# Kernel optimization log

Hardware: AMD Instinct MI355X
Metric: run time of the kernel (lower is better)

## Reference

```python
import jax, jax.numpy as jnp
import numpy as np

N, D = 1024, 512
BS, N_TEXT, N_VIDEO = 64, 16, 16
BETA = 1.0
N_ITERS = 50


def setup_inputs() -> dict:
    key = jax.random.key(0)
    k1, k2 = jax.random.split(key)
    return {
        "t_prob": jax.random.normal(k1, (N, D), dtype=jnp.float32),
        "v_prob": jax.random.normal(k2, (N, D), dtype=jnp.float32),
        "n": N,
        "bs": BS,
        "n_text": N_TEXT,
        "n_video": N_VIDEO,
    }


def _l2norm(x):
    # matches F.normalize(x, p=2, dim=1) (eps irrelevant for randn inputs)
    return x / jnp.linalg.norm(x, axis=1, keepdims=True)


def reference(t_prob, v_prob, n, bs, n_text, n_video):
    dt = t_prob.dtype
    x = _l2norm(t_prob)
    y = _l2norm(v_prob)
    C = 1.0 - x @ y.T                      # [n, n] cosine distance
    A = jnp.exp(-C / BETA)

    sigma0 = jnp.ones((n, 1), dtype=dt) / n
    T0 = jnp.ones((n, n), dtype=dt)

    def step(carry, _):
        T, sigma = carry
        Q = A * T                          # [n, n]
        delta = 1.0 / (n * (Q @ sigma))    # [n, 1]
        sigma_new = 1.0 / (n * (Q.T @ delta))  # [n, 1]
        # diag(delta) @ Q @ diag(sigma) == row/col rescale
        T_new = delta * Q * sigma_new.T
        return (T_new, sigma_new), None

    (T, _), _ = jax.lax.scan(step, (T0, sigma0), None, length=N_ITERS)

    distance_matrix = C.T @ T              # [n, n]
    distance_matrix = distance_matrix.reshape(bs, n_text, bs, n_video).mean(axis=(1, 3))
    dis_loss = jnp.trace(distance_matrix)
    return distance_matrix, dis_loss
```

## Files before the change

kernel.cpp:

```cpp
#include <hip/hip_runtime.h>
#include <math.h>


#define NWG 32
#define TPB 256
#define NIT 50
#define NREP 4

typedef unsigned long long ull;

constexpr int CL_OFF   = 0;
constexpr int CVEC_OFF = 1024 * 1024;
constexpr int CNT_OFF  = CVEC_OFF + 3 * NREP * 1024;

__global__ __launch_bounds__(256) void k_gemm(const float* __restrict__ X,
                                              const float* __restrict__ Y,
                                              float* __restrict__ ws) {
    __shared__ float As[32][68];
    __shared__ float Bs[32][68];
    __shared__ float nX[64], nY[64];
    float* Cl = ws + CL_OFF;

    int tid = threadIdx.x;
    int tx = tid & 15, ty = tid >> 4;
    int bx = blockIdx.x, by = blockIdx.y;
    int lr0 = tid >> 3;
    int kq  = (tid & 7) * 4;

    float acc[4][4] = {};
    float sx0 = 0.f, sx1 = 0.f, sy0 = 0.f, sy1 = 0.f;
    for (int k0 = 0; k0 < 512; k0 += 32) {
        float4 xa = *(const float4*)(X + (size_t)(by * 64 + lr0) * 512 + k0 + kq);
        float4 xb = *(const float4*)(X + (size_t)(by * 64 + lr0 + 32) * 512 + k0 + kq);
        float4 ya = *(const float4*)(Y + (size_t)(bx * 64 + lr0) * 512 + k0 + kq);
        float4 yb = *(const float4*)(Y + (size_t)(bx * 64 + lr0 + 32) * 512 + k0 + kq);
        sx0 += xa.x * xa.x + xa.y * xa.y + xa.z * xa.z + xa.w * xa.w;
        sx1 += xb.x * xb.x + xb.y * xb.y + xb.z * xb.z + xb.w * xb.w;
        sy0 += ya.x * ya.x + ya.y * ya.y + ya.z * ya.z + ya.w * ya.w;
        sy1 += yb.x * yb.x + yb.y * yb.y + yb.z * yb.z + yb.w * yb.w;
        As[kq + 0][lr0] = xa.x; As[kq + 1][lr0] = xa.y;
        As[kq + 2][lr0] = xa.z; As[kq + 3][lr0] = xa.w;
        As[kq + 0][lr0 + 32] = xb.x; As[kq + 1][lr0 + 32] = xb.y;
        As[kq + 2][lr0 + 32] = xb.z; As[kq + 3][lr0 + 32] = xb.w;
        Bs[kq + 0][lr0] = ya.x; Bs[kq + 1][lr0] = ya.y;
        Bs[kq + 2][lr0] = ya.z; Bs[kq + 3][lr0] = ya.w;
        Bs[kq + 0][lr0 + 32] = yb.x; Bs[kq + 1][lr0 + 32] = yb.y;
        Bs[kq + 2][lr0 + 32] = yb.z; Bs[kq + 3][lr0 + 32] = yb.w;
        __syncthreads();
#pragma unroll
        for (int kk = 0; kk < 32; ++kk) {
            float4 a4 = *(const float4*)&As[kk][4 * ty];
            float4 b4 = *(const float4*)&Bs[kk][4 * tx];
            float av[4] = {a4.x, a4.y, a4.z, a4.w};
            float bv[4] = {b4.x, b4.y, b4.z, b4.w};
#pragma unroll
            for (int r = 0; r < 4; ++r)
#pragma unroll
                for (int q = 0; q < 4; ++q) acc[r][q] += av[r] * bv[q];
        }
        __syncthreads();
    }
#pragma unroll
    for (int m = 1; m < 8; m <<= 1) {
        sx0 += __shfl_xor(sx0, m, 64);
        sx1 += __shfl_xor(sx1, m, 64);
        sy0 += __shfl_xor(sy0, m, 64);
        sy1 += __shfl_xor(sy1, m, 64);
    }
    if ((tid & 7) == 0) {
        nX[lr0] = sx0; nX[lr0 + 32] = sx1;
        nY[lr0] = sy0; nY[lr0 + 32] = sy1;
    }
    __syncthreads();

    int i0 = by * 64 + 4 * ty, j0 = bx * 64 + 4 * tx;
    float vy[4];
#pragma unroll
    for (int q = 0; q < 4; ++q) vy[q] = 1.0f / sqrtf(nY[4 * tx + q]);
#pragma unroll
    for (int r = 0; r < 4; ++r) {
        float vx = 1.0f / sqrtf(nX[4 * ty + r]);
        float4 o;
        o.x = acc[r][0] * vx * vy[0] - 1.0f;
        o.y = acc[r][1] * vx * vy[1] - 1.0f;
        o.z = acc[r][2] * vx * vy[2] - 1.0f;
        o.w = acc[r][3] * vx * vy[3] - 1.0f;
        *(float4*)(Cl + (size_t)(i0 + r) * 1024 + j0) = o;
    }
}

__global__ __launch_bounds__(256, 1) void k_ipot(float* __restrict__ ws,
                                                 float* __restrict__ out) {
    __shared__ float sL[1024];
    __shared__ float aL[32];
    __shared__ float buf[4 * 1024];
    __shared__ float twv[4];

    const int g = blockIdx.x, tid = threadIdx.x;
    const int rs = tid >> 6, lane = tid & 63;
    float* Cl   = ws + CL_OFF;
    float* cvec = ws + CVEC_OFF;
    unsigned* grp = (unsigned*)(ws + CNT_OFF);

    float C[8][16], E[8][16];
#pragma unroll
    for (int i = 0; i < 8; ++i) {
        const float* src = Cl + (size_t)(g * 32 + rs * 8 + i) * 1024 + lane * 16;
#pragma unroll
        for (int q = 0; q < 4; ++q) {
            float4 c = *(const float4*)(src + 4 * q);
            C[i][4 * q + 0] = c.x; C[i][4 * q + 1] = c.y;
            C[i][4 * q + 2] = c.z; C[i][4 * q + 3] = c.w;
        }
    }
#pragma unroll
    for (int i = 0; i < 8; ++i)
#pragma unroll
        for (int u = 0; u < 16; ++u) E[i][u] = __expf(C[i][u]);

    float bv[4] = {1.0f, 1.0f, 1.0f, 1.0f};

    for (int t = 0; t < NIT; ++t) {
        if (t == 0) {
            *(float4*)&sL[4 * tid] =
                make_float4(1/1024.f, 1/1024.f, 1/1024.f, 1/1024.f);
        } else {
            if (tid == 0) {
                unsigned tgt = (unsigned)t * 8u;
                long gd = 0;
                while (__hip_atomic_load(&grp[0], __ATOMIC_RELAXED, __HIP_MEMORY_SCOPE_AGENT) < tgt ||
                       __hip_atomic_load(&grp[1], __ATOMIC_RELAXED, __HIP_MEMORY_SCOPE_AGENT) < tgt ||
                       __hip_atomic_load(&grp[2], __ATOMIC_RELAXED, __HIP_MEMORY_SCOPE_AGENT) < tgt ||
                       __hip_atomic_load(&grp[3], __ATOMIC_RELAXED, __HIP_MEMORY_SCOPE_AGENT) < tgt) {
                    __builtin_amdgcn_s_sleep(1);
                    if (++gd > 2000000) break;
                }
            }
            __syncthreads();
            const ull* rb = (const ull*)(cvec + ((t + 2) % 3) * (NREP * 1024)) + 2 * tid;
            ull u00 = __hip_atomic_load(rb + 0 * 512,     __ATOMIC_RELAXED, __HIP_MEMORY_SCOPE_AGENT);
            ull u01 = __hip_atomic_load(rb + 0 * 512 + 1, __ATOMIC_RELAXED, __HIP_MEMORY_SCOPE_AGENT);
            ull u10 = __hip_atomic_load(rb + 1 * 512,     __ATOMIC_RELAXED, __HIP_MEMORY_SCOPE_AGENT);
            ull u11 = __hip_atomic_load(rb + 1 * 512 + 1, __ATOMIC_RELAXED, __HIP_MEMORY_SCOPE_AGENT);
            ull u20 = __hip_atomic_load(rb + 2 * 512,     __ATOMIC_RELAXED, __HIP_MEMORY_SCOPE_AGENT);
            ull u21 = __hip_atomic_load(rb + 2 * 512 + 1, __ATOMIC_RELAXED, __HIP_MEMORY_SCOPE_AGENT);
            ull u30 = __hip_atomic_load(rb + 3 * 512,     __ATOMIC_RELAXED, __HIP_MEMORY_SCOPE_AGENT);
            ull u31 = __hip_atomic_load(rb + 3 * 512 + 1, __ATOMIC_RELAXED, __HIP_MEMORY_SCOPE_AGENT);
            if (t >= 2 && tid < 64) {
                ull* zb = (ull*)(cvec + ((t + 1) % 3) * (NREP * 1024)) + g * 64 + tid;
                __hip_atomic_store(zb, 0ull, __ATOMIC_RELAXED, __HIP_MEMORY_SCOPE_AGENT);
            }
            float c0 = __uint_as_float((unsigned)u00) + __uint_as_float((unsigned)u10) +
                       __uint_as_float((unsigned)u20) + __uint_as_float((unsigned)u30);
            float c1 = __uint_as_float((unsigned)(u00 >> 32)) + __uint_as_float((unsigned)(u10 >> 32)) +
                       __uint_as_float((unsigned)(u20 >> 32)) + __uint_as_float((unsigned)(u30 >> 32));
            float c2 = __uint_as_float((unsigned)u01) + __uint_as_float((unsigned)u11) +
                       __uint_as_float((unsigned)u21) + __uint_as_float((unsigned)u31);
            float c3 = __uint_as_float((unsigned)(u01 >> 32)) + __uint_as_float((unsigned)(u11 >> 32)) +
                       __uint_as_float((unsigned)(u21 >> 32)) + __uint_as_float((unsigned)(u31 >> 32));
            float b0 = 1.0f / c0, b1 = 1.0f / c1, b2 = 1.0f / c2, b3 = 1.0f / c3;
            float4 sn;
            sn.x = b0 * b0 / bv[0] * (1.0f / 1024.0f); bv[0] = b0;
            sn.y = b1 * b1 / bv[1] * (1.0f / 1024.0f); bv[1] = b1;
            sn.z = b2 * b2 / bv[2] * (1.0f / 1024.0f); bv[2] = b2;
            sn.w = b3 * b3 / bv[3] * (1.0f / 1024.0f); bv[3] = b3;
            *(float4*)&sL[4 * tid] = sn;
        }
        __syncthreads();

        float sv[16];
#pragma unroll
        for (int q = 0; q < 4; ++q) {
            float4 s4 = *(const float4*)&sL[lane * 16 + 4 * q];
            sv[4 * q + 0] = s4.x; sv[4 * q + 1] = s4.y;
            sv[4 * q + 2] = s4.z; sv[4 * q + 3] = s4.w;
        }
        float rp[8];
#pragma unroll
        for (int i = 0; i < 8; ++i) {
            float a = 0.0f;
#pragma unroll
            for (int u = 0; u < 16; ++u) a += E[i][u] * sv[u];
            rp[i] = a;
        }
#pragma unroll
        for (int m = 1; m < 64; m <<= 1)
#pragma unroll
            for (int i = 0; i < 8; ++i) rp[i] += __shfl_xor(rp[i], m, 64);
        if (lane == 0) {
#pragma unroll
            for (int i = 0; i < 8; ++i)
                aL[rs * 8 + i] = 1.0f / (1024.0f * rp[i]);
        }
        __syncthreads();

        float av[8];
#pragma unroll
        for (int i = 0; i < 8; ++i) av[i] = aL[rs * 8 + i];
        float cp[16];
#pragma unroll
        for (int u = 0; u < 16; ++u) {
            float a = 0.0f;
#pragma unroll
            for (int i = 0; i < 8; ++i) a += E[i][u] * av[i];
            cp[u] = a;
        }
#pragma unroll
        for (int q = 0; q < 4; ++q)
            *(float4*)&buf[rs * 1024 + lane * 16 + 4 * q] =
                make_float4(cp[4*q], cp[4*q+1], cp[4*q+2], cp[4*q+3]);
        __syncthreads();

        float4 t0 = *(const float4*)&buf[0 * 1024 + 4 * tid];
        float4 t1 = *(const float4*)&buf[1 * 1024 + 4 * tid];
        float4 t2 = *(const float4*)&buf[2 * 1024 + 4 * tid];
        float4 t3 = *(const float4*)&buf[3 * 1024 + 4 * tid];
        float* wb = cvec + (t % 3) * (NREP * 1024) + (g & 3) * 1024 + 4 * tid;
        atomicAdd(wb + 0, t0.x + t1.x + t2.x + t3.x);
        atomicAdd(wb + 1, t0.y + t1.y + t2.y + t3.y);
        atomicAdd(wb + 2, t0.z + t1.z + t2.z + t3.z);
        atomicAdd(wb + 3, t0.w + t1.w + t2.w + t3.w);
        __syncthreads();
        if (tid == 0)
            __hip_atomic_fetch_add(&grp[g >> 3], 1u, __ATOMIC_RELAXED,
                                   __HIP_MEMORY_SCOPE_AGENT);

        if (t < NIT - 1) {
            const float kf = (float)(t + 2);
#pragma unroll
            for (int i = 0; i < 8; ++i)
#pragma unroll
                for (int u = 0; u < 16; ++u) E[i][u] = __expf(kf * C[i][u]);
        }
    }

    if (tid == 0) {
        unsigned tgt = (unsigned)NIT * 8u;
        long gd = 0;
        while (__hip_atomic_load(&grp[0], __ATOMIC_RELAXED, __HIP_MEMORY_SCOPE_AGENT) < tgt ||
               __hip_atomic_load(&grp[1], __ATOMIC_RELAXED, __HIP_MEMORY_SCOPE_AGENT) < tgt ||
               __hip_atomic_load(&grp[2], __ATOMIC_RELAXED, __HIP_MEMORY_SCOPE_AGENT) < tgt ||
               __hip_atomic_load(&grp[3], __ATOMIC_RELAXED, __HIP_MEMORY_SCOPE_AGENT) < tgt) {
            __builtin_amdgcn_s_sleep(1);
            if (++gd > 2000000) break;
        }
    }
    __syncthreads();
    {
        const ull* rb = (const ull*)(cvec + ((NIT - 1) % 3) * (NREP * 1024)) + 2 * tid;
        ull u00 = __hip_atomic_load(rb + 0 * 512,     __ATOMIC_RELAXED, __HIP_MEMORY_SCOPE_AGENT);
        ull u01 = __hip_atomic_load(rb + 0 * 512 + 1, __ATOMIC_RELAXED, __HIP_MEMORY_SCOPE_AGENT);
        ull u10 = __hip_atomic_load(rb + 1 * 512,     __ATOMIC_RELAXED, __HIP_MEMORY_SCOPE_AGENT);
        ull u11 = __hip_atomic_load(rb + 1 * 512 + 1, __ATOMIC_RELAXED, __HIP_MEMORY_SCOPE_AGENT);
        ull u20 = __hip_atomic_load(rb + 2 * 512,     __ATOMIC_RELAXED, __HIP_MEMORY_SCOPE_AGENT);
        ull u21 = __hip_atomic_load(rb + 2 * 512 + 1, __ATOMIC_RELAXED, __HIP_MEMORY_SCOPE_AGENT);
        ull u30 = __hip_atomic_load(rb + 3 * 512,     __ATOMIC_RELAXED, __HIP_MEMORY_SCOPE_AGENT);
        ull u31 = __hip_atomic_load(rb + 3 * 512 + 1, __ATOMIC_RELAXED, __HIP_MEMORY_SCOPE_AGENT);
        float4 bb;
        bb.x = 1.0f / (__uint_as_float((unsigned)u00) + __uint_as_float((unsigned)u10) +
                       __uint_as_float((unsigned)u20) + __uint_as_float((unsigned)u30));
        bb.y = 1.0f / (__uint_as_float((unsigned)(u00 >> 32)) + __uint_as_float((unsigned)(u10 >> 32)) +
                       __uint_as_float((unsigned)(u20 >> 32)) + __uint_as_float((unsigned)(u30 >> 32)));
        bb.z = 1.0f / (__uint_as_float((unsigned)u01) + __uint_as_float((unsigned)u11) +
                       __uint_as_float((unsigned)u21) + __uint_as_float((unsigned)u31));
        bb.w = 1.0f / (__uint_as_float((unsigned)(u01 >> 32)) + __uint_as_float((unsigned)(u11 >> 32)) +
                       __uint_as_float((unsigned)(u21 >> 32)) + __uint_as_float((unsigned)(u31 >> 32)));
        *(float4*)&sL[4 * tid] = bb;
    }
    __syncthreads();

    float* Ps = buf;
    float* Rs = buf + 2048;
    float bl[16];
#pragma unroll
    for (int q = 0; q < 4; ++q) {
        float4 b4 = *(const float4*)&sL[lane * 16 + 4 * q];
        bl[4 * q + 0] = b4.x; bl[4 * q + 1] = b4.y;
        bl[4 * q + 2] = b4.z; bl[4 * q + 3] = b4.w;
    }
#pragma unroll
    for (int i = 0; i < 8; ++i) {
        float p = 0.0f, r = 0.0f;
#pragma unroll
        for (int u = 0; u < 16; ++u) {
            p += C[i][u];
            r += E[i][u] * bl[u];
        }
        Ps[(rs * 8 + i) * 64 + lane] = -p;
        Rs[(rs * 8 + i) * 64 + lane] = aL[rs * 8 + i] * r;
    }
    __syncthreads();

    float Rk[32];
#pragma unroll
    for (int k = 0; k < 32; ++k) Rk[k] = Rs[k * 64 + lane];
    const float sc = 1.0f / (256.0f * 1024.0f);
    float tsum = 0.0f;
#pragma unroll
    for (int q = 0; q < 16; ++q) {
        int o = tid + 256 * q;
        int A = o >> 6;
        float acc = 0.0f;
#pragma unroll
        for (int k = 0; k < 32; ++k) acc += Ps[k * 64 + A] * Rk[k];
        float val = acc * sc;
        atomicAdd(out + o, val);
        if (A == lane) tsum += val;
    }
#pragma unroll
    for (int m = 1; m < 64; m <<= 1) tsum += __shfl_xor(tsum, m, 64);
    if (lane == 0) twv[rs] = tsum;
    __syncthreads();
    if (tid == 0) atomicAdd(out + 4096, twv[0] + twv[1] + twv[2] + twv[3]);
}

extern "C" void kernel_launch(void* const* d_in, const int* in_sizes, int n_in,
                              void* d_out, int out_size, void* d_ws, size_t ws_size,
                              hipStream_t stream) {
    const float* X = (const float*)d_in[0];
    const float* Y = (const float*)d_in[1];
    float* out = (float*)d_out;
    float* ws  = (float*)d_ws;

    (void)hipMemsetAsync((char*)d_ws + (size_t)CVEC_OFF * 4, 0,
                         (3 * NREP * 1024 + 16) * 4, stream);
    (void)hipMemsetAsync(d_out, 0, (size_t)out_size * 4, stream);

    k_gemm<<<dim3(16, 16), 256, 0, stream>>>(X, Y, ws);
    k_ipot<<<NWG, TPB, 0, stream>>>(ws, out);
}
```

Before: 334.2 us.

## Remap IPOT thread ownership to columns and replace per-iteration exp with multiply

Each thread now owns a 4-column strip across all 32 rows instead of 8 rows by 16 columns. Column partial sums therefore come straight from registers into the atomics, with no shared-memory cross-warp reduction or the extra barriers it needed. Row sums now use a wave shuffle plus a small shared reduction. The per-iteration recomputation exp(k*C) is replaced by a running product E *= exp(C). This removes 128 exps per thread per iteration but may accumulate rounding error and raises register pressure (E1, E, Pp). All threads now spin on the grid counters instead of only thread 0, and the spin timeout is raised.

```diff
diff --git a/kernel.cpp b/kernel.cpp
--- a/kernel.cpp
+++ b/kernel.cpp
@@ -89,152 +89,127 @@
     }
 }
 
+__device__ __forceinline__ float f_lo(ull u) { return __uint_as_float((unsigned)u); }
+__device__ __forceinline__ float f_hi(ull u) { return __uint_as_float((unsigned)(u >> 32)); }
+
 __global__ __launch_bounds__(256, 1) void k_ipot(float* __restrict__ ws,
                                                  float* __restrict__ out) {
-    __shared__ float sL[1024];
-    __shared__ float aL[32];
-    __shared__ float buf[4 * 1024];
+    __shared__ float rws[4][32];
+    __shared__ float aLs[32];
+    __shared__ float PsRs[4096];
     __shared__ float twv[4];
 
     const int g = blockIdx.x, tid = threadIdx.x;
     const int rs = tid >> 6, lane = tid & 63;
+    const int j0 = rs * 256 + lane * 4;
     float* Cl   = ws + CL_OFF;
     float* cvec = ws + CVEC_OFF;
     unsigned* grp = (unsigned*)(ws + CNT_OFF);
 
-    float C[8][16], E[8][16];
-#pragma unroll
-    for (int i = 0; i < 8; ++i) {
-        const float* src = Cl + (size_t)(g * 32 + rs * 8 + i) * 1024 + lane * 16;
-#pragma unroll
-        for (int q = 0; q < 4; ++q) {
-            float4 c = *(const float4*)(src + 4 * q);
-            C[i][4 * q + 0] = c.x; C[i][4 * q + 1] = c.y;
-            C[i][4 * q + 2] = c.z; C[i][4 * q + 3] = c.w;
-        }
-    }
-#pragma unroll
-    for (int i = 0; i < 8; ++i)
-#pragma unroll
-        for (int u = 0; u < 16; ++u) E[i][u] = __expf(C[i][u]);
-
+    float E1[32][4], E[32][4], Pp[32];
+#pragma unroll
+    for (int i = 0; i < 32; ++i) {
+        float4 c = *(const float4*)(Cl + (size_t)(g * 32 + i) * 1024 + j0);
+        Pp[i] = c.x + c.y + c.z + c.w;
+        E1[i][0] = __expf(c.x); E1[i][1] = __expf(c.y);
+        E1[i][2] = __expf(c.z); E1[i][3] = __expf(c.w);
+        E[i][0] = E1[i][0]; E[i][1] = E1[i][1];
+        E[i][2] = E1[i][2]; E[i][3] = E1[i][3];
+    }
     float bv[4] = {1.0f, 1.0f, 1.0f, 1.0f};
+    float al[32];
 
     for (int t = 0; t < NIT; ++t) {
+        float s0, s1, s2, s3;
         if (t == 0) {
-            *(float4*)&sL[4 * tid] =
-                make_float4(1/1024.f, 1/1024.f, 1/1024.f, 1/1024.f);
+            s0 = s1 = s2 = s3 = 1.0f / 1024.0f;
         } else {
-            if (tid == 0) {
-                unsigned tgt = (unsigned)t * 8u;
-                long gd = 0;
-                while (__hip_atomic_load(&grp[0], __ATOMIC_RELAXED, __HIP_MEMORY_SCOPE_AGENT) < tgt ||
-                       __hip_atomic_load(&grp[1], __ATOMIC_RELAXED, __HIP_MEMORY_SCOPE_AGENT) < tgt ||
-                       __hip_atomic_load(&grp[2], __ATOMIC_RELAXED, __HIP_MEMORY_SCOPE_AGENT) < tgt ||
-                       __hip_atomic_load(&grp[3], __ATOMIC_RELAXED, __HIP_MEMORY_SCOPE_AGENT) < tgt) {
-                    __builtin_amdgcn_s_sleep(1);
-                    if (++gd > 2000000) break;
-                }
+            unsigned tgt = (unsigned)t * 8u;
+            long gd = 0;
+            while (__hip_atomic_load(&grp[0], __ATOMIC_RELAXED, __HIP_MEMORY_SCOPE_AGENT) < tgt ||
+                   __hip_atomic_load(&grp[1], __ATOMIC_RELAXED, __HIP_MEMORY_SCOPE_AGENT) < tgt ||
+                   __hip_atomic_load(&grp[2], __ATOMIC_RELAXED, __HIP_MEMORY_SCOPE_AGENT) < tgt ||
+                   __hip_atomic_load(&grp[3], __ATOMIC_RELAXED, __HIP_MEMORY_SCOPE_AGENT) < tgt) {
+                __builtin_amdgcn_s_sleep(1);
+                if (++gd > 3000000) break;
             }
-            __syncthreads();
-            const ull* rb = (const ull*)(cvec + ((t + 2) % 3) * (NREP * 1024)) + 2 * tid;
-            ull u00 = __hip_atomic_load(rb + 0 * 512,     __ATOMIC_RELAXED, __HIP_MEMORY_SCOPE_AGENT);
-            ull u01 = __hip_atomic_load(rb + 0 * 512 + 1, __ATOMIC_RELAXED, __HIP_MEMORY_SCOPE_AGENT);
-            ull u10 = __hip_atomic_load(rb + 1 * 512,     __ATOMIC_RELAXED, __HIP_MEMORY_SCOPE_AGENT);
-            ull u11 = __hip_atomic_load(rb + 1 * 512 + 1, __ATOMIC_RELAXED, __HIP_MEMORY_SCOPE_AGENT);
-            ull u20 = __hip_atomic_load(rb + 2 * 512,     __ATOMIC_RELAXED, __HIP_MEMORY_SCOPE_AGENT);
-            ull u21 = __hip_atomic_load(rb + 2 * 512 + 1, __ATOMIC_RELAXED, __HIP_MEMORY_SCOPE_AGENT);
-            ull u30 = __hip_atomic_load(rb + 3 * 512,     __ATOMIC_RELAXED, __HIP_MEMORY_SCOPE_AGENT);
-            ull u31 = __hip_atomic_load(rb + 3 * 512 + 1, __ATOMIC_RELAXED, __HIP_MEMORY_SCOPE_AGENT);
+            const ull* rb = (const ull*)(cvec + ((t + 2) % 3) * (NREP * 1024)) + (j0 >> 1);
+            ull a0 = __hip_atomic_load(rb + 0,    __ATOMIC_RELAXED, __HIP_MEMORY_SCOPE_AGENT);
+            ull a1 = __hip_atomic_load(rb + 1,    __ATOMIC_RELAXED, __HIP_MEMORY_SCOPE_AGENT);
+            ull b0 = __hip_atomic_load(rb + 512,  __ATOMIC_RELAXED, __HIP_MEMORY_SCOPE_AGENT);
+            ull b1 = __hip_atomic_load(rb + 513,  __ATOMIC_RELAXED, __HIP_MEMORY_SCOPE_AGENT);
+            ull c0 = __hip_atomic_load(rb + 1024, __ATOMIC_RELAXED, __HIP_MEMORY_SCOPE_AGENT);
+            ull c1 = __hip_atomic_load(rb + 1025, __ATOMIC_RELAXED, __HIP_MEMORY_SCOPE_AGENT);
+            ull d0 = __hip_atomic_load(rb + 1536, __ATOMIC_RELAXED, __HIP_MEMORY_SCOPE_AGENT);
+            ull d1 = __hip_atomic_load(rb + 1537, __ATOMIC_RELAXED, __HIP_MEMORY_SCOPE_AGENT);
             if (t >= 2 && tid < 64) {
                 ull* zb = (ull*)(cvec + ((t + 1) % 3) * (NREP * 1024)) + g * 64 + tid;
                 __hip_atomic_store(zb, 0ull, __ATOMIC_RELAXED, __HIP_MEMORY_SCOPE_AGENT);
             }
-            float c0 = __uint_as_float((unsigned)u00) + __uint_as_float((unsigned)u10) +
-                       __uint_as_float((unsigned)u20) + __uint_as_float((unsigned)u30);
-            float c1 = __uint_as_float((unsigned)(u00 >> 32)) + __uint_as_float((unsigned)(u10 >> 32)) +
-                       __uint_as_float((unsigned)(u20 >> 32)) + __uint_as_float((unsigned)(u30 >> 32));
-            float c2 = __uint_as_float((unsigned)u01) + __uint_as_float((unsigned)u11) +
-                       __uint_as_float((unsigned)u21) + __uint_as_float((unsigned)u31);
-            float c3 = __uint_as_float((unsigned)(u01 >> 32)) + __uint_as_float((unsigned)(u11 >> 32)) +
-                       __uint_as_float((unsigned)(u21 >> 32)) + __uint_as_float((unsigned)(u31 >> 32));
-            float b0 = 1.0f / c0, b1 = 1.0f / c1, b2 = 1.0f / c2, b3 = 1.0f / c3;
-            float4 sn;
-            sn.x = b0 * b0 / bv[0] * (1.0f / 1024.0f); bv[0] = b0;
-            sn.y = b1 * b1 / bv[1] * (1.0f / 1024.0f); bv[1] = b1;
-            sn.z = b2 * b2 / bv[2] * (1.0f / 1024.0f); bv[2] = b2;
-            sn.w = b3 * b3 / bv[3] * (1.0f / 1024.0f); bv[3] = b3;
-            *(float4*)&sL[4 * tid] = sn;
-        }
-        __syncthreads();
-
-        float sv[16];
-#pragma unroll
-        for (int q = 0; q < 4; ++q) {
-            float4 s4 = *(const float4*)&sL[lane * 16 + 4 * q];
-            sv[4 * q + 0] = s4.x; sv[4 * q + 1] = s4.y;
-            sv[4 * q + 2] = s4.z; sv[4 * q + 3] = s4.w;
-        }
-        float rp[8];
-#pragma unroll
-        for (int i = 0; i < 8; ++i) {
-            float a = 0.0f;
-#pragma unroll
-            for (int u = 0; u < 16; ++u) a += E[i][u] * sv[u];
-            rp[i] = a;
-        }
+            float cc0 = f_lo(a0) + f_lo(b0) + f_lo(c0) + f_lo(d0);
+            float cc1 = f_hi(a0) + f_hi(b0) + f_hi(c0) + f_hi(d0);
+            float cc2 = f_lo(a1) + f_lo(b1) + f_lo(c1) + f_lo(d1);
+            float cc3 = f_hi(a1) + f_hi(b1) + f_hi(c1) + f_hi(d1);
+            float nb0 = 1.0f / cc0, nb1 = 1.0f / cc1;
+            float nb2 = 1.0f / cc2, nb3 = 1.0f / cc3;
+            s0 = nb0 * nb0 / bv[0] * (1.0f / 1024.0f); bv[0] = nb0;
+            s1 = nb1 * nb1 / bv[1] * (1.0f / 1024.0f); bv[1] = nb1;
+            s2 = nb2 * nb2 / bv[2] * (1.0f / 1024.0f); bv[2] = nb2;
+            s3 = nb3 * nb3 / bv[3] * (1.0f / 1024.0f); bv[3] = nb3;
+        }
+
+        float rp[32];
+#pragma unroll
+        for (int i = 0; i < 32; ++i)
+            rp[i] = E[i][0] * s0 + E[i][1] * s1 + E[i][2] * s2 + E[i][3] * s3;
 #pragma unroll
         for (int m = 1; m < 64; m <<= 1)
 #pragma unroll
-            for (int i = 0; i < 8; ++i) rp[i] += __shfl_xor(rp[i], m, 64);
+            for (int i = 0; i < 32; ++i) rp[i] += __shfl_xor(rp[i], m, 64);
         if (lane == 0) {
 #pragma unroll
-            for (int i = 0; i < 8; ++i)
-                aL[rs * 8 + i] = 1.0f / (1024.0f * rp[i]);
-        }
-        __syncthreads();
-
-        float av[8];
-#pragma unroll
-        for (int i = 0; i < 8; ++i) av[i] = aL[rs * 8 + i];
-        float cp[16];
-#pragma unroll
-        for (int u = 0; u < 16; ++u) {
-            float a = 0.0f;
-#pragma unroll
-            for (int i = 0; i < 8; ++i) a += E[i][u] * av[i];
-            cp[u] = a;
-        }
-#pragma unroll
-        for (int q = 0; q < 4; ++q)
-            *(float4*)&buf[rs * 1024 + lane * 16 + 4 * q] =
-                make_float4(cp[4*q], cp[4*q+1], cp[4*q+2], cp[4*q+3]);
-        __syncthreads();
-
-        float4 t0 = *(const float4*)&buf[0 * 1024 + 4 * tid];
-        float4 t1 = *(const float4*)&buf[1 * 1024 + 4 * tid];
-        float4 t2 = *(const float4*)&buf[2 * 1024 + 4 * tid];
-        float4 t3 = *(const float4*)&buf[3 * 1024 + 4 * tid];
-        float* wb = cvec + (t % 3) * (NREP * 1024) + (g & 3) * 1024 + 4 * tid;
-        atomicAdd(wb + 0, t0.x + t1.x + t2.x + t3.x);
-        atomicAdd(wb + 1, t0.y + t1.y + t2.y + t3.y);
-        atomicAdd(wb + 2, t0.z + t1.z + t2.z + t3.z);
-        atomicAdd(wb + 3, t0.w + t1.w + t2.w + t3.w);
+            for (int q = 0; q < 8; ++q)
+                *(float4*)&rws[rs][4 * q] =
+                    make_float4(rp[4*q], rp[4*q+1], rp[4*q+2], rp[4*q+3]);
+        }
+        __syncthreads();
+        if (tid < 32)
+            aLs[tid] = 1.0f / (1024.0f * (rws[0][tid] + rws[1][tid] +
+                                          rws[2][tid] + rws[3][tid]));
+        __syncthreads();
+#pragma unroll
+        for (int q = 0; q < 8; ++q) {
+            float4 a4 = *(const float4*)&aLs[4 * q];
+            al[4*q] = a4.x; al[4*q+1] = a4.y; al[4*q+2] = a4.z; al[4*q+3] = a4.w;
+        }
+
+        float p0 = 0.f, p1 = 0.f, p2 = 0.f, p3 = 0.f;
+#pragma unroll
+        for (int i = 0; i < 32; ++i) {
+            float ai = al[i];
+            p0 += E[i][0] * ai; p1 += E[i][1] * ai;
+            p2 += E[i][2] * ai; p3 += E[i][3] * ai;
+        }
+        float* wb = cvec + (t % 3) * (NREP * 1024) + (g & 3) * 1024 + j0;
+        atomicAdd(wb + 0, p0);
+        atomicAdd(wb + 1, p1);
+        atomicAdd(wb + 2, p2);
+        atomicAdd(wb + 3, p3);
         __syncthreads();
         if (tid == 0)
             __hip_atomic_fetch_add(&grp[g >> 3], 1u, __ATOMIC_RELAXED,
                                    __HIP_MEMORY_SCOPE_AGENT);
 
         if (t < NIT - 1) {
-            const float kf = (float)(t + 2);
-#pragma unroll
-            for (int i = 0; i < 8; ++i)
-#pragma unroll
-                for (int u = 0; u < 16; ++u) E[i][u] = __expf(kf * C[i][u]);
-        }
-    }
-
-    if (tid == 0) {
+#pragma unroll
+            for (int i = 0; i < 32; ++i) {
+                E[i][0] *= E1[i][0]; E[i][1] *= E1[i][1];
+                E[i][2] *= E1[i][2]; E[i][3] *= E1[i][3];
+            }
+        }
+    }
+
+    {
         unsigned tgt = (unsigned)NIT * 8u;
         long gd = 0;
         while (__hip_atomic_load(&grp[0], __ATOMIC_RELAXED, __HIP_MEMORY_SCOPE_AGENT) < tgt ||
@@ -242,52 +217,49 @@
                __hip_atomic_load(&grp[2], __ATOMIC_RELAXED, __HIP_MEMORY_SCOPE_AGENT) < tgt ||
                __hip_atomic_load(&grp[3], __ATOMIC_RELAXED, __HIP_MEMORY_SCOPE_AGENT) < tgt) {
             __builtin_amdgcn_s_sleep(1);
-            if (++gd > 2000000) break;
-        }
-    }
-    __syncthreads();
+            if (++gd > 3000000) break;
+        }
+    }
+    float bl[4];
     {
-        const ull* rb = (const ull*)(cvec + ((NIT - 1) % 3) * (NREP * 1024)) + 2 * tid;
-        ull u00 = __hip_atomic_load(rb + 0 * 512,     __ATOMIC_RELAXED, __HIP_MEMORY_SCOPE_AGENT);
-        ull u01 = __hip_atomic_load(rb + 0 * 512 + 1, __ATOMIC_RELAXED, __HIP_MEMORY_SCOPE_AGENT);
-        ull u10 = __hip_atomic_load(rb + 1 * 512,     __ATOMIC_RELAXED, __HIP_MEMORY_SCOPE_AGENT);
-        ull u11 = __hip_atomic_load(rb + 1 * 512 + 1, __ATOMIC_RELAXED, __HIP_MEMORY_SCOPE_AGENT);
-        ull u20 = __hip_atomic_load(rb + 2 * 512,     __ATOMIC_RELAXED, __HIP_MEMORY_SCOPE_AGENT);
-        ull u21 = __hip_atomic_load(rb + 2 * 512 + 1, __ATOMIC_RELAXED, __HIP_MEMORY_SCOPE_AGENT);
-        ull u30 = __hip_atomic_load(rb + 3 * 512,     __ATOMIC_RELAXED, __HIP_MEMORY_SCOPE_AGENT);
-        ull u31 = __hip_atomic_load(rb + 3 * 512 + 1, __ATOMIC_RELAXED, __HIP_MEMORY_SCOPE_AGENT);
-        float4 bb;
-        bb.x = 1.0f / (__uint_as_float((unsigned)u00) + __uint_as_float((unsigned)u10) +
-                       __uint_as_float((unsigned)u20) + __uint_as_float((unsigned)u30));
-        bb.y = 1.0f / (__uint_as_float((unsigned)(u00 >> 32)) + __uint_as_float((unsigned)(u10 >> 32)) +
-                       __uint_as_float((unsigned)(u20 >> 32)) + __uint_as_float((unsigned)(u30 >> 32)));
-        bb.z = 1.0f / (__uint_as_float((unsigned)u01) + __uint_as_float((unsigned)u11) +
-                       __uint_as_float((unsigned)u21) + __uint_as_float((unsigned)u31));
-        bb.w = 1.0f / (__uint_as_float((unsigned)(u01 >> 32)) + __uint_as_float((unsigned)(u11 >> 32)) +
-                       __uint_as_float((unsigned)(u21 >> 32)) + __uint_as_float((unsigned)(u31 >> 32)));
-        *(float4*)&sL[4 * tid] = bb;
-    }
-    __syncthreads();
-
-    float* Ps = buf;
-    float* Rs = buf + 2048;
-    float bl[16];
-#pragma unroll
-    for (int q = 0; q < 4; ++q) {
-        float4 b4 = *(const float4*)&sL[lane * 16 + 4 * q];
-        bl[4 * q + 0] = b4.x; bl[4 * q + 1] = b4.y;
-        bl[4 * q + 2] = b4.z; bl[4 * q + 3] = b4.w;
-    }
-#pragma unroll
-    for (int i = 0; i < 8; ++i) {
-        float p = 0.0f, r = 0.0f;
-#pragma unroll
-        for (int u = 0; u < 16; ++u) {
-            p += C[i][u];
-            r += E[i][u] * bl[u];
-        }
-        Ps[(rs * 8 + i) * 64 + lane] = -p;
-        Rs[(rs * 8 + i) * 64 + lane] = aL[rs * 8 + i] * r;
+        const ull* rb = (const ull*)(cvec + ((NIT - 1) % 3) * (NREP * 1024)) + (j0 >> 1);
+        ull a0 = __hip_atomic_load(rb + 0,    __ATOMIC_RELAXED, __HIP_MEMORY_SCOPE_AGENT);
+        ull a1 = __hip_atomic_load(rb + 1,    __ATOMIC_RELAXED, __HIP_MEMORY_SCOPE_AGENT);
+        ull b0 = __hip_atomic_load(rb + 512,  __ATOMIC_RELAXED, __HIP_MEMORY_SCOPE_AGENT);
+        ull b1 = __hip_atomic_load(rb + 513,  __ATOMIC_RELAXED, __HIP_MEMORY_SCOPE_AGENT);
+        ull c0 = __hip_atomic_load(rb + 1024, __ATOMIC_RELAXED, __HIP_MEMORY_SCOPE_AGENT);
+        ull c1 = __hip_atomic_load(rb + 1025, __ATOMIC_RELAXED, __HIP_MEMORY_SCOPE_AGENT);
+        ull d0 = __hip_atomic_load(rb + 1536, __ATOMIC_RELAXED, __HIP_MEMORY_SCOPE_AGENT);
+        ull d1 = __hip_atomic_load(rb + 1537, __ATOMIC_RELAXED, __HIP_MEMORY_SCOPE_AGENT);
+        bl[0] = 1.0f / (f_lo(a0) + f_lo(b0) + f_lo(c0) + f_lo(d0));
+        bl[1] = 1.0f / (f_hi(a0) + f_hi(b0) + f_hi(c0) + f_hi(d0));
+        bl[2] = 1.0f / (f_lo(a1) + f_lo(b1) + f_lo(c1) + f_lo(d1));
+        bl[3] = 1.0f / (f_hi(a1) + f_hi(b1) + f_hi(c1) + f_hi(d1));
+    }
+
+    float* Ps = PsRs;
+    float* Rs = PsRs + 2048;
+    float Pl[32], Rl[32];
+#pragma unroll
+    for (int k = 0; k < 32; ++k) {
+        Pl[k] = Pp[k];
+        Rl[k] = E[k][0] * bl[0] + E[k][1] * bl[1] +
+                E[k][2] * bl[2] + E[k][3] * bl[3];
+    }
+#pragma unroll
+    for (int m = 1; m < 4; m <<= 1)
+#pragma unroll
+        for (int k = 0; k < 32; ++k) {
+            Pl[k] += __shfl_xor(Pl[k], m, 64);
+            Rl[k] += __shfl_xor(Rl[k], m, 64);
+        }
+    if ((lane & 3) == 0) {
+        int A = rs * 16 + (lane >> 2);
+#pragma unroll
+        for (int k = 0; k < 32; ++k) {
+            Ps[k * 64 + A] = -Pl[k];
+            Rs[k * 64 + A] = al[k] * Rl[k];
+        }
     }
     __syncthreads();
 
@@ -299,7 +271,7 @@
 #pragma unroll
     for (int q = 0; q < 16; ++q) {
         int o = tid + 256 * q;
-        int A = o >> 6;
+        int A = 4 * q + rs;
         float acc = 0.0f;
 #pragma unroll
         for (int k = 0; k < 32; ++k) acc += Ps[k * 64 + A] * Rk[k];
```

Result: slower. 375.4 us (+12.3%).
